# Optimization experiments

Measured on AMD Instinct MI355X. Metric: run time of the kernel, lower is better.

## Reference

```python
import jax, jax.numpy as jnp
import numpy as np

# Standard Human3.6M 17-joint skeleton parents; CHILD_JOINTS[j] = children of joint j.
_PARENTS = np.array([-1, 0, 1, 2, 0, 4, 5, 0, 7, 8, 9, 8, 11, 12, 8, 14, 15])
_J = 17

def _child_mean_matrix():
    """[J,J] matrix M s.t. child_feat = M @ x_joints reproduces the per-joint
    child-mean gather loop (identity row for leaf joints)."""
    M = np.zeros((_J, _J), dtype=np.float32)
    for j in range(_J):
        ch = [i for i in range(_J) if _PARENTS[i] == j]
        if ch:
            M[j, ch] = 1.0 / len(ch)
        else:
            M[j, j] = 1.0
    return M

_CHILD_M = _child_mean_matrix()

B, N, J, C = 8, 243, 17, 512
H = 8
D = C // H

def setup_inputs() -> dict:
    key = jax.random.key(0)
    ks = jax.random.split(key, 9)
    s = 0.02
    return {
        "x": jax.random.normal(ks[0], (B, N, J, C), dtype=jnp.float32),
        "W_qkv": jax.random.normal(ks[1], (C, 3 * C), dtype=jnp.float32) * s,
        "b_qkv": jnp.zeros((3 * C,), dtype=jnp.float32),
        "W_q": jax.random.normal(ks[2], (C, C), dtype=jnp.float32) * s,
        "b_q": jnp.zeros((C,), dtype=jnp.float32),
        "W_kv": jax.random.normal(ks[3], (C, 2 * C), dtype=jnp.float32) * s,
        "b_kv": jnp.zeros((2 * C,), dtype=jnp.float32),
        "W_proj": jax.random.normal(ks[4], (C, C), dtype=jnp.float32) * s,
        "b_proj": jnp.zeros((C,), dtype=jnp.float32),
    }

def _attn(q, k, v, scale):
    # q,k,v: [B,J,N,H,D]; attention over temporal axis N per (b,j,h)
    a = jnp.einsum('bjnhd,bjmhd->bjhnm', q, k) * scale
    a = jax.nn.softmax(a, axis=-1)
    return jnp.einsum('bjhnm,bjmhd->bjnhd', a, v)

def reference(x, W_qkv, b_qkv, W_q, b_q, W_kv, b_kv, W_proj, b_proj):
    Bx, Nx, Jx, Cx = x.shape
    scale = 1.0 / jnp.sqrt(jnp.asarray(D, x.dtype))
    Mchild = jnp.asarray(_CHILD_M, x.dtype)

    xt = jnp.transpose(x, (0, 2, 1, 3))  # [B,J,N,C] -> per-(b,j) temporal sequences

    # Temporal self-attention (TSA)
    qkv = (xt @ W_qkv + b_qkv).reshape(Bx, Jx, Nx, 3, H, D)
    q_t, k_t, v_t = qkv[:, :, :, 0], qkv[:, :, :, 1], qkv[:, :, :, 2]
    x_tsa = _attn(q_t, k_t, v_t, scale).reshape(Bx, Jx, Nx, Cx)

    # Hierarchical temporal cross-attention (HTC): K/V from child-joint mean
    child = jnp.einsum('jk,bknc->bjnc', Mchild, xt)  # [B,J,N,C]
    q_h = (xt @ W_q + b_q).reshape(Bx, Jx, Nx, H, D)
    kv = (child @ W_kv + b_kv).reshape(Bx, Jx, Nx, 2, H, D)
    k_h, v_h = kv[:, :, :, 0], kv[:, :, :, 1]
    x_htc = _attn(q_h, k_h, v_h, scale).reshape(Bx, Jx, Nx, Cx)

    # Fuse, project, residual + LayerNorm (no affine; dropout is identity in eval)
    fuse = jnp.transpose(x_tsa + x_htc, (0, 2, 1, 3))  # [B,N,J,C]
    fuse = fuse @ W_proj + b_proj
    y = x + fuse
    mu = jnp.mean(y, axis=-1, keepdims=True)
    var = jnp.var(y, axis=-1, keepdims=True)
    return (y - mu) / jnp.sqrt(var + 1e-5)
```

## Files before the change

kernel.cpp:

```cpp
#include <hip/hip_runtime.h>

typedef unsigned short u16;
typedef unsigned int u32;
typedef __attribute__((ext_vector_type(8))) short bf16x8;
typedef __attribute__((ext_vector_type(8))) u16  u16x8;
typedef __attribute__((ext_vector_type(4))) float f32x4;

#define TOK   33048
#define NSEQ  243
#define TE    16920576u
#define GSTR  15552
#define VTP   256

__device__ __forceinline__ float bf2f(u16 u){
    union { unsigned int i; float f; } v; v.i = ((unsigned int)u) << 16; return v.f;
}
__device__ __forceinline__ u16 f2bf(float f){
    union { float f; unsigned int i; } v; v.f = f;
    unsigned int r = v.i + 0x7fffu + ((v.i >> 16) & 1u);
    return (u16)(r >> 16);
}

__device__ __forceinline__ void gload_lds16(const void* g, void* l){
    __builtin_amdgcn_global_load_lds(
        (const __attribute__((address_space(1))) unsigned int*)g,
        (__attribute__((address_space(3))) unsigned int*)l, 16, 0, 0);
}

__global__ __launch_bounds__(256) void k_cvt_xbf(const float* __restrict__ x, u16* __restrict__ xbf){
    int idx = blockIdx.x*256 + threadIdx.x;
    int t  = idx >> 6;
    int c8 = (idx & 63) << 3;
    unsigned b   = (unsigned)t / 4131u;
    unsigned rem = (unsigned)t % 4131u;
    unsigned j = rem / 243u, n = rem % 243u;
    const float* src = x + ((size_t)(b*243u + n)*17u + j)*512u + c8;
    f32x4 a = *(const f32x4*)src;
    f32x4 c = *(const f32x4*)(src+4);
    u16x8 o;
    #pragma unroll
    for (int e=0;e<4;e++){ o[e]=f2bf(a[e]); o[e+4]=f2bf(c[e]); }
    *(u16x8*)(xbf + (size_t)t*512 + c8) = o;
}

__global__ __launch_bounds__(256) void k_cvt_wcat(const float* __restrict__ Wqkv,
                                                  const float* __restrict__ Wq,
                                                  const float* __restrict__ Wkv,
                                                  u16* __restrict__ WcatT){
    int idx = blockIdx.x*256 + threadIdx.x;
    int k  = idx / 384;
    int c0 = (idx % 384) * 8;
    const float* src;
    if (c0 < 1536)      src = Wqkv + (size_t)k*1536 + c0;
    else if (c0 < 2048) src = Wq   + (size_t)k*512  + (c0 - 1536);
    else                src = Wkv  + (size_t)k*1024 + (c0 - 2048);
    f32x4 a = *(const f32x4*)src;
    f32x4 b = *(const f32x4*)(src+4);
    #pragma unroll
    for (int e=0;e<4;e++){
        WcatT[(size_t)(c0+e)*512 + k]   = f2bf(a[e]);
        WcatT[(size_t)(c0+4+e)*512 + k] = f2bf(b[e]);
    }
}

__global__ __launch_bounds__(256) void k_cvt_wproj(const float* __restrict__ Wp, u16* __restrict__ WpT){
    int idx = blockIdx.x*256 + threadIdx.x;
    int k  = idx / 64;
    int c0 = (idx % 64) * 8;
    f32x4 a = *(const f32x4*)(Wp + (size_t)k*512 + c0);
    f32x4 b = *(const f32x4*)(Wp + (size_t)k*512 + c0 + 4);
    #pragma unroll
    for (int e=0;e<4;e++){
        WpT[(size_t)(c0+e)*512 + k]   = f2bf(a[e]);
        WpT[(size_t)(c0+4+e)*512 + k] = f2bf(b[e]);
    }
}

__global__ __launch_bounds__(256) void k_gemm_in(
    const u16* __restrict__ xbf, const u16* __restrict__ WcatT,
    const float* __restrict__ b_qkv, const float* __restrict__ b_q,
    const float* __restrict__ b_kv, u16* __restrict__ ws3, int c_off)
{
    __shared__ __align__(16) u16 smem[32768];

    const int orig = blockIdx.x;
    const int xcd  = orig & 7;
    const int wg   = (xcd < 4 ? xcd*389 : 4*389 + (xcd-4)*388) + (orig >> 3);
    const int nt = wg % 12, mt = wg / 12;

    const int tid = threadIdx.x;
    const int w = tid >> 6, lane = tid & 63;
    const int wm = w >> 1, wn = w & 1;
    const int lg = lane >> 4, li = lane & 15;
    const int x7 = li & 7;

    const int sr8  = lane >> 3;
    const int schx = (lane & 7) ^ sr8;
    const u16* gA = xbf   + (size_t)(mt*128 + w*32 + sr8)*512 + schx*8;
    const u16* gB = WcatT + (size_t)(c_off + nt*128 + w*32 + sr8)*512 + schx*8;

    f32x4 acc[4][4];
    #pragma unroll
    for (int i=0;i<4;i++)
        #pragma unroll
        for (int jj=0;jj<4;jj++){ acc[i][jj][0]=0.f; acc[i][jj][1]=0.f; acc[i][jj][2]=0.f; acc[i][jj][3]=0.f; }

    #pragma unroll
    for (int i=0;i<4;i++){
        gload_lds16(gA + i*4096, smem + (w*32 + i*8)*64);
        gload_lds16(gB + i*4096, smem + 8192 + (w*32 + i*8)*64);
    }

    int cur = 0;
    #pragma unroll
    for (int k0 = 0; k0 < 512; k0 += 64){
        if (k0 < 448){
            u16* nb = smem + (cur^1)*16384;
            #pragma unroll
            for (int i=0;i<4;i++){
                gload_lds16(gA + i*4096 + k0 + 64, nb + (w*32 + i*8)*64);
                gload_lds16(gB + i*4096 + k0 + 64, nb + 8192 + (w*32 + i*8)*64);
            }
            asm volatile("s_waitcnt vmcnt(8)");
        } else {
            asm volatile("s_waitcnt vmcnt(0)");
        }
        __builtin_amdgcn_s_barrier();
        const u16* As = smem + cur*16384;
        const u16* Bs = As + 8192;
        #pragma unroll
        for (int ks=0; ks<2; ks++){
            bf16x8 av[4], bv[4];
            #pragma unroll
            for (int mf=0;mf<4;mf++){
                const int R = wm*64 + mf*16 + li;
                av[mf] = *(const bf16x8*)&As[R*64 + (((ks*4+lg) ^ x7)*8)];
            }
            #pragma unroll
            for (int nf=0;nf<4;nf++){
                const int R = wn*64 + nf*16 + li;
                bv[nf] = *(const bf16x8*)&Bs[R*64 + (((ks*4+lg) ^ x7)*8)];
            }
            #pragma unroll
            for (int mf=0;mf<4;mf++)
                #pragma unroll
                for (int nf=0;nf<4;nf++)
                    acc[mf][nf] = __builtin_amdgcn_mfma_f32_16x16x32_bf16(av[mf], bv[nf], acc[mf][nf], 0, 0, 0);
        }
        __builtin_amdgcn_s_barrier();
        cur ^= 1;
    }

    float bias[4];
    #pragma unroll
    for (int nf=0;nf<4;nf++){
        const int c = c_off + nt*128 + wn*64 + nf*16 + li;
        bias[nf] = (c < 1536) ? b_qkv[c] : (c < 2048 ? b_q[c-1536] : b_kv[c-2048]);
    }

    u16* L = smem + w*1152;
    const int colbase = nt*128 + wn*64;
    const int slot = colbase >> 9;
    const float osc = (slot == 0) ? 0.125f : 1.0f;
    const int hh   = (colbase >> 6) & 7;
    const int rloc = lane & 15;
    const int cchunk = lane >> 4;
    const int dd = (colbase + cchunk*8) & 63;
    u16* tbase = ws3 + (size_t)slot * TE;
    u16* vt    = ws3 + (size_t)2 * TE;

    #pragma unroll
    for (int mf=0;mf<4;mf++){
        __syncthreads();
        #pragma unroll
        for (int nf=0;nf<4;nf++)
            #pragma unroll
            for (int reg=0;reg<4;reg++)
                L[(lg*4+reg)*72 + nf*16 + li] = f2bf((acc[mf][nf][reg] + bias[nf]) * osc);
        __syncthreads();
        const int rr_base = mt*128 + wm*64 + mf*16;
        if (slot < 2){
            const int rr = rr_base + rloc;
            if (rr < TOK){
                u16x8 v0 = *(const u16x8*)&L[rloc*72 + cchunk*8];
                u16x8 v1 = *(const u16x8*)&L[rloc*72 + 32 + cchunk*8];
                const unsigned bj = (unsigned)rr / 243u;
                const unsigned n  = (unsigned)rr % 243u;
                u16* dst = tbase + ((size_t)(bj*8u + hh)*243u + n)*64u + dd;
                *(u16x8*)dst      = v0;
                *(u16x8*)(dst+32) = v1;
            }
        } else {
            u16 colv[16];
            #pragma unroll
            for (int r=0;r<16;r++) colv[r] = L[r*72 + lane];
            if (rr_base < TOK){
                const unsigned bj0 = (unsigned)rr_base / 243u;
                const unsigned n0  = (unsigned)rr_base % 243u;
                if (n0 <= 227 && rr_base + 15 < TOK){
                    u16x8 vlo, vhi;
                    #pragma unroll
                    for (int e=0;e<8;e++){ vlo[e]=colv[e]; vhi[e]=colv[e+8]; }
                    u16* dst = vt + ((size_t)(bj0*8u + hh)*64u + lane)*VTP + n0;
                    *(u16x8*)dst     = vlo;
                    *(u16x8*)(dst+8) = vhi;
                } else {
                    for (int r=0;r<16;r++){
                        const int rr = rr_base + r;
                        if (rr < TOK){
                            const unsigned bjr = (unsigned)rr / 243u;
                            const unsigned nr  = (unsigned)rr % 243u;
                            vt[((size_t)(bjr*8u + hh)*64u + lane)*VTP + nr] = colv[r];
                        }
                    }
                }
            }
        }
    }
}

__constant__ int g_child[17][3] = {
  {1,4,7},{2,-1,-1},{3,-1,-1},{3,-1,-1},{5,-1,-1},{6,-1,-1},{6,-1,-1},{8,-1,-1},
  {9,11,14},{10,-1,-1},{10,-1,-1},{12,-1,-1},{13,-1,-1},{13,-1,-1},{15,-1,-1},
  {16,-1,-1},{16,-1,-1}};
__constant__ float g_cw[17] = {0.33333333f,1,1,1,1,1,1,1,0.33333333f,1,1,1,1,1,1,1,1};

__global__ __launch_bounds__(256) void k_mixk(const u16* __restrict__ Kraw, u16* __restrict__ Kmix){
    const int c = blockIdx.x*256 + threadIdx.x;
    const int g = c / 1944;
    const int off = (c % 1944) * 8;
    const int bj = g >> 3, h = g & 7;
    const int b_ = bj / 17, j_ = bj % 17;
    const float wgt = g_cw[j_];
    float acc[8];
    #pragma unroll
    for (int e=0;e<8;e++) acc[e]=0.f;
    #pragma unroll
    for (int ci=0;ci<3;ci++){
        const int cj = g_child[j_][ci];
        if (cj >= 0){
            const u16x8 v = *(const u16x8*)(Kraw + (size_t)((b_*17+cj)*8+h)*GSTR + off);
            #pragma unroll
            for (int e=0;e<8;e++) acc[e] += wgt*bf2f(v[e]);
        }
    }
    u16x8 o;
    #pragma unroll
    for (int e=0;e<8;e++) o[e]=f2bf(acc[e]);
    *(u16x8*)(Kmix + (size_t)g*GSTR + off) = o;
}

__global__ __launch_bounds__(256) void k_mixv(const u16* __restrict__ VTraw, u16* __restrict__ VTmix){
    const int c = blockIdx.x*256 + threadIdx.x;
    const int g = c / 2048;
    const int off = (c % 2048) * 8;
    const int bj = g >> 3, h = g & 7;
    const int b_ = bj / 17, j_ = bj % 17;
    const float wgt = g_cw[j_];
    float acc[8];
    #pragma unroll
    for (int e=0;e<8;e++) acc[e]=0.f;
    #pragma unroll
    for (int ci=0;ci<3;ci++){
        const int cj = g_child[j_][ci];
        if (cj >= 0){
            const u16x8 v = *(const u16x8*)(VTraw + (size_t)((b_*17+cj)*8+h)*16384u + off);
            #pragma unroll
            for (int e=0;e<8;e++) acc[e] += wgt*bf2f(v[e]);
        }
    }
    u16x8 o;
    #pragma unroll
    for (int e=0;e<8;e++) o[e]=f2bf(acc[e]);
    *(u16x8*)(VTmix + (size_t)g*16384u + off) = o;
}

__global__ __launch_bounds__(256, 3) void k_attn(
    const u16* __restrict__ Qb, const u16* __restrict__ Kb,
    const u16* __restrict__ VTb, u16* __restrict__ attn, int rmw)
{
    __shared__ __align__(16) u16 smem[16384];

    const int orig = blockIdx.x;
    const int xcd  = orig & 7;
    const int lin  = orig >> 3;
    const int p2   = lin & 1;
    const int g    = (lin >> 1)*8 + xcd;
    const int bj = g >> 3, h = g & 7;

    const int tid = threadIdx.x, lane = tid & 63, w = tid >> 6;
    const int lg = lane >> 4, li = lane & 15;

    const int qrowA = p2*128 + w*16;
    const int qrowB = qrowA + 64;
    bf16x8 qA0 = {0,0,0,0,0,0,0,0}, qA1 = qA0, qB0 = qA0, qB1 = qA0;
    {
        const int qrA = qrowA + li;
        const u16* qp = Qb + (size_t)g*GSTR + (size_t)qrA*64;
        qA0 = *(const bf16x8*)(qp + lg*8);
        qA1 = *(const bf16x8*)(qp + 32 + lg*8);
        const int qrB = qrowB + li;
        if (qrB < NSEQ){
            const u16* qp2 = Qb + (size_t)g*GSTR + (size_t)qrB*64;
            qB0 = *(const bf16x8*)(qp2 + lg*8);
            qB1 = *(const bf16x8*)(qp2 + 32 + lg*8);
        }
    }

    const int schx = (lane & 7) ^ (lane >> 3);
    const u16* ksrc = Kb  + (size_t)g*GSTR   + (size_t)(w*16 + (lane>>3))*64  + schx*8;
    const u16* vsrc = VTb + (size_t)g*16384u + (size_t)(w*16 + (lane>>3))*VTP + schx*8;

    const int laneA = li + 32*(lg & 1);
    const int laneB = laneA + 16;
    const bool sel = (lg >> 1) != 0;
    const int x7 = li & 7;

    float sumA = 0.f, sumB = 0.f;
    f32x4 oA[4], oB[4];
    #pragma unroll
    for (int dn=0;dn<4;dn++){
        oA[dn][0]=0.f; oA[dn][1]=0.f; oA[dn][2]=0.f; oA[dn][3]=0.f;
        oB[dn][0]=0.f; oB[dn][1]=0.f; oB[dn][2]=0.f; oB[dn][3]=0.f;
    }

    {
        char* b0 = (char*)smem;
        gload_lds16(ksrc,         b0 + w*2048);
        gload_lds16(ksrc + 512,   b0 + w*2048 + 1024);
        gload_lds16(vsrc,         b0 + 8192 + w*2048);
        gload_lds16(vsrc + 8*VTP, b0 + 8192 + w*2048 + 1024);
    }

    int cur = 0;
    #pragma unroll
    for (int t=0; t<4; t++){
        if (t < 3){
            char* nb = (char*)smem + (cur^1)*16384;
            gload_lds16(ksrc + (size_t)(t+1)*4096,        nb + w*2048);
            gload_lds16(ksrc + (size_t)(t+1)*4096 + 512,  nb + w*2048 + 1024);
            gload_lds16(vsrc + (t+1)*64,                  nb + 8192 + w*2048);
            gload_lds16(vsrc + (t+1)*64 + 8*VTP,          nb + 8192 + w*2048 + 1024);
            asm volatile("s_waitcnt vmcnt(4)");
        } else {
            asm volatile("s_waitcnt vmcnt(0)");
        }
        __builtin_amdgcn_s_barrier();
        char* kl = (char*)smem + cur*16384;
        char* vl = kl + 8192;

        #pragma unroll
        for (int half=0; half<2; half++){
            u32 lo2A[2], hi2A[2], lo2B[2], hi2B[2];
            #pragma unroll
            for (int t2=0; t2<2; t2++){
                const int nt2l = half*2 + t2;
                const int row  = nt2l*16 + li;
                const bf16x8 kb0 = *(const bf16x8*)(kl + row*128 + (((lg  ) ^ x7)<<4));
                const bf16x8 kb1 = *(const bf16x8*)(kl + row*128 + (((4+lg) ^ x7)<<4));
                f32x4 sA; sA[0]=0.f; sA[1]=0.f; sA[2]=0.f; sA[3]=0.f;
                f32x4 sB = sA;
                sA = __builtin_amdgcn_mfma_f32_16x16x32_bf16(kb0, qA0, sA, 0,0,0);
                sA = __builtin_amdgcn_mfma_f32_16x16x32_bf16(kb1, qA1, sA, 0,0,0);
                sB = __builtin_amdgcn_mfma_f32_16x16x32_bf16(kb0, qB0, sB, 0,0,0);
                sB = __builtin_amdgcn_mfma_f32_16x16x32_bf16(kb1, qB1, sB, 0,0,0);
                if (t == 3 && nt2l == 3){
                    sA[3] = -1e30f; sB[3] = -1e30f;
                    if (lg){ sA[0]=-1e30f; sA[1]=-1e30f; sA[2]=-1e30f;
                             sB[0]=-1e30f; sB[1]=-1e30f; sB[2]=-1e30f; }
                }
                const float a0 = __expf(sA[0]);
                const float a1 = __expf(sA[1]);
                const float a2 = __expf(sA[2]);
                const float a3 = __expf(sA[3]);
                sumA += (a0+a1)+(a2+a3);
                lo2A[t2] = (u32)f2bf(a0) | ((u32)f2bf(a1) << 16);
                hi2A[t2] = (u32)f2bf(a2) | ((u32)f2bf(a3) << 16);
                const float b0 = __expf(sB[0]);
                const float b1 = __expf(sB[1]);
                const float b2 = __expf(sB[2]);
                const float b3 = __expf(sB[3]);
                sumB += (b0+b1)+(b2+b3);
                lo2B[t2] = (u32)f2bf(b0) | ((u32)f2bf(b1) << 16);
                hi2B[t2] = (u32)f2bf(b2) | ((u32)f2bf(b3) << 16);
            }
            bf16x8 paA, paB;
            {
                u32 a0 = __shfl((int)lo2A[0], laneA), a1 = __shfl((int)lo2A[1], laneA);
                u32 b0 = __shfl((int)hi2A[0], laneA), b1 = __shfl((int)hi2A[1], laneA);
                u32 c0 = __shfl((int)lo2A[0], laneB), c1 = __shfl((int)lo2A[1], laneB);
                u32 d0 = __shfl((int)hi2A[0], laneB), d1 = __shfl((int)hi2A[1], laneB);
                union { u32 u[4]; bf16x8 v; } pk;
                pk.u[0] = sel ? a1 : a0;
                pk.u[1] = sel ? b1 : b0;
                pk.u[2] = sel ? c1 : c0;
                pk.u[3] = sel ? d1 : d0;
                paA = pk.v;
            }
            {
                u32 a0 = __shfl((int)lo2B[0], laneA), a1 = __shfl((int)lo2B[1], laneA);
                u32 b0 = __shfl((int)hi2B[0], laneA), b1 = __shfl((int)hi2B[1], laneA);
                u32 c0 = __shfl((int)lo2B[0], laneB), c1 = __shfl((int)lo2B[1], laneB);
                u32 d0 = __shfl((int)hi2B[0], laneB), d1 = __shfl((int)hi2B[1], laneB);
                union { u32 u[4]; bf16x8 v; } pk;
                pk.u[0] = sel ? a1 : a0;
                pk.u[1] = sel ? b1 : b0;
                pk.u[2] = sel ? c1 : c0;
                pk.u[3] = sel ? d1 : d0;
                paB = pk.v;
            }
            #pragma unroll
            for (int dn=0;dn<4;dn++){
                const int d = dn*16 + li;
                const bf16x8 vb = *(const bf16x8*)(vl + d*128 + ((((half<<2)+lg) ^ x7)<<4));
                oA[dn] = __builtin_amdgcn_mfma_f32_16x16x32_bf16(paA, vb, oA[dn], 0,0,0);
                oB[dn] = __builtin_amdgcn_mfma_f32_16x16x32_bf16(paB, vb, oB[dn], 0,0,0);
            }
        }
        __builtin_amdgcn_s_barrier();
        cur ^= 1;
    }

    sumA += __shfl_xor(sumA,16); sumA += __shfl_xor(sumA,32);
    sumB += __shfl_xor(sumB,16); sumB += __shfl_xor(sumB,32);
    const float invA = 1.f/sumA;
    const float invB = 1.f/sumB;
    float invrA[4], invrB[4];
    #pragma unroll
    for (int r=0;r<4;r++){
        invrA[r] = __shfl(invA, lg*4+r);
        invrB[r] = __shfl(invB, lg*4+r);
    }

    #pragma unroll
    for (int dn=0;dn<4;dn++){
        #pragma unroll
        for (int r=0;r<4;r++){
            const int qrow = qrowA + lg*4 + r;
            const size_t off = ((size_t)bj*243 + qrow)*512 + h*64 + dn*16 + li;
            float val = oA[dn][r] * invrA[r];
            if (rmw) val += bf2f(attn[off]);
            attn[off] = f2bf(val);
        }
        #pragma unroll
        for (int r=0;r<4;r++){
            const int qrow = qrowB + lg*4 + r;
            if (qrow < NSEQ){
                const size_t off = ((size_t)bj*243 + qrow)*512 + h*64 + dn*16 + li;
                float val = oB[dn][r] * invrB[r];
                if (rmw) val += bf2f(attn[off]);
                attn[off] = f2bf(val);
            }
        }
    }
}

__global__ __launch_bounds__(256) void k_gemm_proj(
    const u16* __restrict__ attnb, const u16* __restrict__ WprojT,
    const float* __restrict__ b_proj, float* __restrict__ fuse)
{
    __shared__ __align__(16) u16 smem[32768];

    const int orig = blockIdx.x;
    const int xcd  = orig & 7;
    const int wg   = (xcd < 4 ? xcd*130 : 4*130 + (xcd-4)*129) + (orig >> 3);
    const int nt = wg & 3, mt = wg >> 2;

    const int tid = threadIdx.x;
    const int w = tid >> 6, lane = tid & 63;
    const int wm = w >> 1, wn = w & 1;
    const int lg = lane >> 4, li = lane & 15;
    const int x7 = li & 7;

    const int sr8  = lane >> 3;
    const int schx = (lane & 7) ^ sr8;
    const u16* gA = attnb  + (size_t)(mt*128 + w*32 + sr8)*512 + schx*8;
    const u16* gB = WprojT + (size_t)(nt*128 + w*32 + sr8)*512 + schx*8;

    f32x4 acc[4][4];
    #pragma unroll
    for (int i=0;i<4;i++)
        #pragma unroll
        for (int jj=0;jj<4;jj++){ acc[i][jj][0]=0.f; acc[i][jj][1]=0.f; acc[i][jj][2]=0.f; acc[i][jj][3]=0.f; }

    #pragma unroll
    for (int i=0;i<4;i++){
        gload_lds16(gA + i*4096, smem + (w*32 + i*8)*64);
        gload_lds16(gB + i*4096, smem + 8192 + (w*32 + i*8)*64);
    }

    int cur = 0;
    #pragma unroll
    for (int k0 = 0; k0 < 512; k0 += 64){
        if (k0 < 448){
            u16* nb = smem + (cur^1)*16384;
            #pragma unroll
            for (int i=0;i<4;i++){
                gload_lds16(gA + i*4096 + k0 + 64, nb + (w*32 + i*8)*64);
                gload_lds16(gB + i*4096 + k0 + 64, nb + 8192 + (w*32 + i*8)*64);
            }
            asm volatile("s_waitcnt vmcnt(8)");
        } else {
            asm volatile("s_waitcnt vmcnt(0)");
        }
        __builtin_amdgcn_s_barrier();
        const u16* As = smem + cur*16384;
        const u16* Bs = As + 8192;
        #pragma unroll
        for (int ks=0; ks<2; ks++){
            bf16x8 av[4], bv[4];
            #pragma unroll
            for (int mf=0;mf<4;mf++){
                const int R = wm*64 + mf*16 + li;
                av[mf] = *(const bf16x8*)&As[R*64 + (((ks*4+lg) ^ x7)*8)];
            }
            #pragma unroll
            for (int nf=0;nf<4;nf++){
                const int R = wn*64 + nf*16 + li;
                bv[nf] = *(const bf16x8*)&Bs[R*64 + (((ks*4+lg) ^ x7)*8)];
            }
            #pragma unroll
            for (int mf=0;mf<4;mf++)
                #pragma unroll
                for (int nf=0;nf<4;nf++)
                    acc[mf][nf] = __builtin_amdgcn_mfma_f32_16x16x32_bf16(av[mf], bv[nf], acc[mf][nf], 0, 0, 0);
        }
        __builtin_amdgcn_s_barrier();
        cur ^= 1;
    }

    #pragma unroll
    for (int mf=0;mf<4;mf++)
        #pragma unroll
        for (int reg=0;reg<4;reg++){
            const int rr = mt*128 + wm*64 + mf*16 + lg*4 + reg;
            if (rr < TOK){
                #pragma unroll
                for (int nf=0;nf<4;nf++){
                    const int c = nt*128 + wn*64 + nf*16 + li;
                    fuse[(size_t)rr*512 + c] = acc[mf][nf][reg] + b_proj[c];
                }
            }
        }
}

__global__ __launch_bounds__(256) void k_ln(
    const float* __restrict__ x, const float* __restrict__ fuse, float* __restrict__ out)
{
    const int w = threadIdx.x >> 6, lane = threadIdx.x & 63;
    const int o = blockIdx.x*4 + w;
    const unsigned b_  = (unsigned)o / 4131u;
    const unsigned rem = (unsigned)o % 4131u;
    const unsigned n = rem / 17u, j = rem % 17u;
    const unsigned t = (b_*17u + j)*243u + n;
    const float* fr = fuse + (size_t)t*512 + lane*8;
    const float* xr = x    + (size_t)o*512 + lane*8;
    f32x4 f0 = *(const f32x4*)fr, f1 = *(const f32x4*)(fr+4);
    f32x4 x0 = *(const f32x4*)xr, x1 = *(const f32x4*)(xr+4);
    float y[8];
    #pragma unroll
    for (int e=0;e<4;e++){ y[e] = x0[e]+f0[e]; y[e+4] = x1[e]+f1[e]; }
    float s1=0.f, s2=0.f;
    #pragma unroll
    for (int e=0;e<8;e++){ s1 += y[e]; s2 += y[e]*y[e]; }
    #pragma unroll
    for (int m=1;m<64;m<<=1){ s1 += __shfl_xor(s1,m); s2 += __shfl_xor(s2,m); }
    const float mu  = s1 * (1.f/512.f);
    const float var = s2 * (1.f/512.f) - mu*mu;
    const float rstd = rsqrtf(var + 1e-5f);
    float* orow = out + (size_t)o*512 + lane*8;
    f32x4 o0, o1;
    #pragma unroll
    for (int e=0;e<4;e++){ o0[e] = (y[e]-mu)*rstd; o1[e] = (y[e+4]-mu)*rstd; }
    *(f32x4*)orow = o0; *(f32x4*)(orow+4) = o1;
}

extern "C" void kernel_launch(void* const* d_in, const int* in_sizes, int n_in,
                              void* d_out, int out_size, void* d_ws, size_t ws_size,
                              hipStream_t stream)
{
    const float* x      = (const float*)d_in[0];
    const float* W_qkv  = (const float*)d_in[1];
    const float* b_qkv  = (const float*)d_in[2];
    const float* W_q    = (const float*)d_in[3];
    const float* b_q    = (const float*)d_in[4];
    const float* W_kv   = (const float*)d_in[5];
    const float* b_kv   = (const float*)d_in[6];
    const float* W_proj = (const float*)d_in[7];
    const float* b_proj = (const float*)d_in[8];

    char* ws = (char*)d_ws;
    u16*   xbf    = (u16*)(ws);
    u16*   kmix   = (u16*)(ws);
    u16*   ws3    = (u16*)(ws + 33972224u);
    u16*   attn   = (u16*)(ws + 137306112u);
    u16*   WcatT  = (u16*)(ws + 171278336u);
    u16*   WprojT = (u16*)(ws + 174424064u);
    u16*   vtmix  = (u16*)(ws + 174948352u);
    float* fuse   = (float*)(ws + 33972224u);
    float* out    = (float*)d_out;

    k_cvt_xbf  <<<8262, 256, 0, stream>>>(x, xbf);
    k_cvt_wcat <<<768,  256, 0, stream>>>(W_qkv, W_q, W_kv, WcatT);
    k_cvt_wproj<<<128,  256, 0, stream>>>(W_proj, WprojT);

    k_gemm_in<<<3108, 256, 0, stream>>>(xbf, WcatT, b_qkv, b_q, b_kv, ws3, 0);
    k_attn<<<2176, 256, 0, stream>>>(ws3, ws3 + (size_t)TE, ws3 + (size_t)2*TE, attn, 0);

    k_gemm_in<<<3108, 256, 0, stream>>>(xbf, WcatT, b_qkv, b_q, b_kv, ws3, 1536);
    k_mixk<<<8262, 256, 0, stream>>>(ws3 + (size_t)TE, kmix);
    k_mixv<<<8704, 256, 0, stream>>>(ws3 + (size_t)2*TE, vtmix);
    k_attn<<<2176, 256, 0, stream>>>(ws3, kmix, vtmix, attn, 1);

    k_gemm_proj<<<1036, 256, 0, stream>>>(attn, WprojT, b_proj, fuse);

    k_ln<<<8262, 256, 0, stream>>>(x, fuse, out);
}
```

Measured before the change: 370.1 us.

## Load GEMM B operand straight into registers and store projection output as bf16

Both GEMM kernels now read the weight (B) fragments from global memory directly into a double-buffered register array instead of staging them through LDS. This halves LDS use and removes the B LDS reads, so occupancy and LDS bandwidth should improve, at the cost of more VGPRs and uncoalesced global loads per wave. Separately, the projection output is written as bf16 rather than fp32, which halves the write traffic from the projection GEMM and the read traffic into the LayerNorm kernel. The price is a small precision loss in the residual add.

Measured after the change: 497.9 us. +34.6%, slower.

```diff
diff --git a/kernel.cpp b/kernel.cpp
--- a/kernel.cpp
+++ b/kernel.cpp
@@ -81,7 +81,7 @@
     const float* __restrict__ b_qkv, const float* __restrict__ b_q,
     const float* __restrict__ b_kv, u16* __restrict__ ws3, int c_off)
 {
-    __shared__ __align__(16) u16 smem[32768];
+    __shared__ __align__(16) u16 smem[16384];
 
     const int orig = blockIdx.x;
     const int xcd  = orig & 7;
@@ -96,8 +96,8 @@
 
     const int sr8  = lane >> 3;
     const int schx = (lane & 7) ^ sr8;
-    const u16* gA = xbf   + (size_t)(mt*128 + w*32 + sr8)*512 + schx*8;
-    const u16* gB = WcatT + (size_t)(c_off + nt*128 + w*32 + sr8)*512 + schx*8;
+    const u16* gA = xbf + (size_t)(mt*128 + w*32 + sr8)*512 + schx*8;
+    const u16* gBrow = WcatT + (size_t)(c_off + nt*128 + wn*64 + li)*512 + lg*8;
 
     f32x4 acc[4][4];
     #pragma unroll
@@ -105,47 +105,50 @@
         #pragma unroll
         for (int jj=0;jj<4;jj++){ acc[i][jj][0]=0.f; acc[i][jj][1]=0.f; acc[i][jj][2]=0.f; acc[i][jj][3]=0.f; }
 
-    #pragma unroll
-    for (int i=0;i<4;i++){
+    bf16x8 bvbuf[2][8];
+
+    #pragma unroll
+    for (int i=0;i<4;i++)
         gload_lds16(gA + i*4096, smem + (w*32 + i*8)*64);
-        gload_lds16(gB + i*4096, smem + 8192 + (w*32 + i*8)*64);
-    }
+    #pragma unroll
+    for (int ks=0;ks<2;ks++)
+        #pragma unroll
+        for (int nf=0;nf<4;nf++)
+            bvbuf[0][ks*4+nf] = *(const bf16x8*)(gBrow + (size_t)nf*8192 + ks*32);
 
     int cur = 0;
     #pragma unroll
     for (int k0 = 0; k0 < 512; k0 += 64){
+        const int pc = (k0 >> 6) & 1;
         if (k0 < 448){
-            u16* nb = smem + (cur^1)*16384;
-            #pragma unroll
-            for (int i=0;i<4;i++){
+            u16* nb = smem + (cur^1)*8192;
+            #pragma unroll
+            for (int i=0;i<4;i++)
                 gload_lds16(gA + i*4096 + k0 + 64, nb + (w*32 + i*8)*64);
-                gload_lds16(gB + i*4096 + k0 + 64, nb + 8192 + (w*32 + i*8)*64);
-            }
-            asm volatile("s_waitcnt vmcnt(8)");
+            asm volatile("s_waitcnt vmcnt(4)");
+            #pragma unroll
+            for (int ks=0;ks<2;ks++)
+                #pragma unroll
+                for (int nf=0;nf<4;nf++)
+                    bvbuf[pc^1][ks*4+nf] = *(const bf16x8*)(gBrow + (size_t)nf*8192 + k0 + 64 + ks*32);
         } else {
             asm volatile("s_waitcnt vmcnt(0)");
         }
         __builtin_amdgcn_s_barrier();
-        const u16* As = smem + cur*16384;
-        const u16* Bs = As + 8192;
+        const u16* As = smem + cur*8192;
         #pragma unroll
         for (int ks=0; ks<2; ks++){
-            bf16x8 av[4], bv[4];
+            bf16x8 av[4];
             #pragma unroll
             for (int mf=0;mf<4;mf++){
                 const int R = wm*64 + mf*16 + li;
                 av[mf] = *(const bf16x8*)&As[R*64 + (((ks*4+lg) ^ x7)*8)];
             }
             #pragma unroll
-            for (int nf=0;nf<4;nf++){
-                const int R = wn*64 + nf*16 + li;
-                bv[nf] = *(const bf16x8*)&Bs[R*64 + (((ks*4+lg) ^ x7)*8)];
-            }
-            #pragma unroll
             for (int mf=0;mf<4;mf++)
                 #pragma unroll
                 for (int nf=0;nf<4;nf++)
-                    acc[mf][nf] = __builtin_amdgcn_mfma_f32_16x16x32_bf16(av[mf], bv[nf], acc[mf][nf], 0, 0, 0);
+                    acc[mf][nf] = __builtin_amdgcn_mfma_f32_16x16x32_bf16(av[mf], bvbuf[pc][ks*4+nf], acc[mf][nf], 0, 0, 0);
         }
         __builtin_amdgcn_s_barrier();
         cur ^= 1;
@@ -457,9 +460,9 @@
 
 __global__ __launch_bounds__(256) void k_gemm_proj(
     const u16* __restrict__ attnb, const u16* __restrict__ WprojT,
-    const float* __restrict__ b_proj, float* __restrict__ fuse)
+    const float* __restrict__ b_proj, u16* __restrict__ fuseb)
 {
-    __shared__ __align__(16) u16 smem[32768];
+    __shared__ __align__(16) u16 smem[16384];
 
     const int orig = blockIdx.x;
     const int xcd  = orig & 7;
@@ -474,8 +477,8 @@
 
     const int sr8  = lane >> 3;
     const int schx = (lane & 7) ^ sr8;
-    const u16* gA = attnb  + (size_t)(mt*128 + w*32 + sr8)*512 + schx*8;
-    const u16* gB = WprojT + (size_t)(nt*128 + w*32 + sr8)*512 + schx*8;
+    const u16* gA = attnb + (size_t)(mt*128 + w*32 + sr8)*512 + schx*8;
+    const u16* gBrow = WprojT + (size_t)(nt*128 + wn*64 + li)*512 + lg*8;
 
     f32x4 acc[4][4];
     #pragma unroll
@@ -483,47 +486,50 @@
         #pragma unroll
         for (int jj=0;jj<4;jj++){ acc[i][jj][0]=0.f; acc[i][jj][1]=0.f; acc[i][jj][2]=0.f; acc[i][jj][3]=0.f; }
 
-    #pragma unroll
-    for (int i=0;i<4;i++){
+    bf16x8 bvbuf[2][8];
+
+    #pragma unroll
+    for (int i=0;i<4;i++)
         gload_lds16(gA + i*4096, smem + (w*32 + i*8)*64);
-        gload_lds16(gB + i*4096, smem + 8192 + (w*32 + i*8)*64);
-    }
+    #pragma unroll
+    for (int ks=0;ks<2;ks++)
+        #pragma unroll
+        for (int nf=0;nf<4;nf++)
+            bvbuf[0][ks*4+nf] = *(const bf16x8*)(gBrow + (size_t)nf*8192 + ks*32);
 
     int cur = 0;
     #pragma unroll
     for (int k0 = 0; k0 < 512; k0 += 64){
+        const int pc = (k0 >> 6) & 1;
         if (k0 < 448){
-            u16* nb = smem + (cur^1)*16384;
-            #pragma unroll
-            for (int i=0;i<4;i++){
+            u16* nb = smem + (cur^1)*8192;
+            #pragma unroll
+            for (int i=0;i<4;i++)
                 gload_lds16(gA + i*4096 + k0 + 64, nb + (w*32 + i*8)*64);
-                gload_lds16(gB + i*4096 + k0 + 64, nb + 8192 + (w*32 + i*8)*64);
-            }
-            asm volatile("s_waitcnt vmcnt(8)");
+            asm volatile("s_waitcnt vmcnt(4)");
+            #pragma unroll
+            for (int ks=0;ks<2;ks++)
+                #pragma unroll
+                for (int nf=0;nf<4;nf++)
+                    bvbuf[pc^1][ks*4+nf] = *(const bf16x8*)(gBrow + (size_t)nf*8192 + k0 + 64 + ks*32);
         } else {
             asm volatile("s_waitcnt vmcnt(0)");
         }
         __builtin_amdgcn_s_barrier();
-        const u16* As = smem + cur*16384;
-        const u16* Bs = As + 8192;
+        const u16* As = smem + cur*8192;
         #pragma unroll
         for (int ks=0; ks<2; ks++){
-            bf16x8 av[4], bv[4];
+            bf16x8 av[4];
             #pragma unroll
             for (int mf=0;mf<4;mf++){
                 const int R = wm*64 + mf*16 + li;
                 av[mf] = *(const bf16x8*)&As[R*64 + (((ks*4+lg) ^ x7)*8)];
             }
             #pragma unroll
-            for (int nf=0;nf<4;nf++){
-                const int R = wn*64 + nf*16 + li;
-                bv[nf] = *(const bf16x8*)&Bs[R*64 + (((ks*4+lg) ^ x7)*8)];
-            }
-            #pragma unroll
             for (int mf=0;mf<4;mf++)
                 #pragma unroll
                 for (int nf=0;nf<4;nf++)
-                    acc[mf][nf] = __builtin_amdgcn_mfma_f32_16x16x32_bf16(av[mf], bv[nf], acc[mf][nf], 0, 0, 0);
+                    acc[mf][nf] = __builtin_amdgcn_mfma_f32_16x16x32_bf16(av[mf], bvbuf[pc][ks*4+nf], acc[mf][nf], 0, 0, 0);
         }
         __builtin_amdgcn_s_barrier();
         cur ^= 1;
@@ -538,14 +544,14 @@
                 #pragma unroll
                 for (int nf=0;nf<4;nf++){
                     const int c = nt*128 + wn*64 + nf*16 + li;
-                    fuse[(size_t)rr*512 + c] = acc[mf][nf][reg] + b_proj[c];
+                    fuseb[(size_t)rr*512 + c] = f2bf(acc[mf][nf][reg] + b_proj[c]);
                 }
             }
         }
 }
 
 __global__ __launch_bounds__(256) void k_ln(
-    const float* __restrict__ x, const float* __restrict__ fuse, float* __restrict__ out)
+    const float* __restrict__ x, const u16* __restrict__ fuseb, float* __restrict__ out)
 {
     const int w = threadIdx.x >> 6, lane = threadIdx.x & 63;
     const int o = blockIdx.x*4 + w;
@@ -553,13 +559,13 @@
     const unsigned rem = (unsigned)o % 4131u;
     const unsigned n = rem / 17u, j = rem % 17u;
     const unsigned t = (b_*17u + j)*243u + n;
-    const float* fr = fuse + (size_t)t*512 + lane*8;
-    const float* xr = x    + (size_t)o*512 + lane*8;
-    f32x4 f0 = *(const f32x4*)fr, f1 = *(const f32x4*)(fr+4);
+    const u16*   fr = fuseb + (size_t)t*512 + lane*8;
+    const float* xr = x     + (size_t)o*512 + lane*8;
+    u16x8 f = *(const u16x8*)fr;
     f32x4 x0 = *(const f32x4*)xr, x1 = *(const f32x4*)(xr+4);
     float y[8];
     #pragma unroll
-    for (int e=0;e<4;e++){ y[e] = x0[e]+f0[e]; y[e+4] = x1[e]+f1[e]; }
+    for (int e=0;e<4;e++){ y[e] = x0[e]+bf2f(f[e]); y[e+4] = x1[e]+bf2f(f[e+4]); }
     float s1=0.f, s2=0.f;
     #pragma unroll
     for (int e=0;e<8;e++){ s1 += y[e]; s2 += y[e]*y[e]; }
@@ -597,7 +603,7 @@
     u16*   WcatT  = (u16*)(ws + 171278336u);
     u16*   WprojT = (u16*)(ws + 174424064u);
     u16*   vtmix  = (u16*)(ws + 174948352u);
-    float* fuse   = (float*)(ws + 33972224u);
+    u16*   fuseb  = (u16*)(ws + 33972224u);
     float* out    = (float*)d_out;
 
     k_cvt_xbf  <<<8262, 256, 0, stream>>>(x, xbf);
@@ -612,7 +618,7 @@
     k_mixv<<<8704, 256, 0, stream>>>(ws3 + (size_t)2*TE, vtmix);
     k_attn<<<2176, 256, 0, stream>>>(ws3, kmix, vtmix, attn, 1);
 
-    k_gemm_proj<<<1036, 256, 0, stream>>>(attn, WprojT, b_proj, fuse);
-
-    k_ln<<<8262, 256, 0, stream>>>(x, fuse, out);
-}
+    k_gemm_proj<<<1036, 256, 0, stream>>>(attn, WprojT, b_proj, fuseb);
+
+    k_ln<<<8262, 256, 0, stream>>>(x, fuseb, out);
+}
```
